# Optimization experiments

Measured on AMD Instinct MI355X. Metric: run time of the kernel, lower is better.

## Reference

```python
import jax, jax.numpy as jnp
import numpy as np

DIM = 96
SHIFT_SIZE = 3
EPS = 1e-5


def conv1x1(x, w, b):
    # x: [B,C,H,W], w: [O,C], b: [O]
    return jnp.einsum('bchw,oc->bohw', x, w) + b[None, :, None, None]


def group_norm1(x, gamma, beta):
    # GroupNorm with 1 group: normalize over (C,H,W) per sample
    mean = jnp.mean(x, axis=(1, 2, 3), keepdims=True)
    var = jnp.var(x, axis=(1, 2, 3), keepdims=True)
    xn = (x - mean) * jax.lax.rsqrt(var + EPS)
    return xn * gamma[None, :, None, None] + beta[None, :, None, None]


def axial_shift(x, shift_size, axis, sign=1):
    # pad -> chunk channels -> roll each chunk -> cat -> narrow (zero-fill shift)
    B, C, H, W = x.shape
    p = shift_size // 2
    xp = jnp.pad(x, ((0, 0), (0, 0), (p, p), (p, p)))
    chunks = jnp.split(xp, shift_size, axis=1)
    rolled = [jnp.roll(c, sign * s, axis=axis) for c, s in zip(chunks, range(-p, p + 1))]
    xc = jnp.concatenate(rolled, axis=1)
    return xc[:, :, p:p + H, p:p + W]


def setup_inputs() -> dict:
    key = jax.random.key(0)
    ks = jax.random.split(key, 13)
    B, C, H, W = 4, DIM, 256, 256
    s = 1.0 / np.sqrt(C)
    inp = {
        'x': jax.random.normal(ks[0], (B, C, H, W), jnp.float32),
        'w1': jax.random.uniform(ks[1], (C, C), jnp.float32, -s, s),
        'b1': jax.random.uniform(ks[2], (C,), jnp.float32, -s, s),
        'w21': jax.random.uniform(ks[3], (C, C), jnp.float32, -s, s),
        'b21': jax.random.uniform(ks[4], (C,), jnp.float32, -s, s),
        'w22': jax.random.uniform(ks[5], (C, C), jnp.float32, -s, s),
        'b22': jax.random.uniform(ks[6], (C,), jnp.float32, -s, s),
        'w3': jax.random.uniform(ks[7], (C, C), jnp.float32, -s, s),
        'b3': jax.random.uniform(ks[8], (C,), jnp.float32, -s, s),
        'gn1_w': jnp.ones((C,), jnp.float32),
        'gn1_b': jnp.zeros((C,), jnp.float32),
        'gn2_w': jnp.ones((C,), jnp.float32),
        'gn2_b': jnp.zeros((C,), jnp.float32),
    }
    return inp


def reference(x, w1, b1, w21, b21, w22, b22, w3, b3, gn1_w, gn1_b, gn2_w, gn2_b):
    gelu = lambda t: jax.nn.gelu(t, approximate=False)  # torch nn.GELU default (erf)
    x = gelu(group_norm1(conv1x1(x, w1, b1), gn1_w, gn1_b))
    x_lr = axial_shift(x, SHIFT_SIZE, axis=3)
    x_l_diag = axial_shift(x_lr, SHIFT_SIZE, axis=2)
    x_td = axial_shift(x, SHIFT_SIZE, axis=2)
    x_r_diag = axial_shift(x_td, SHIFT_SIZE, axis=3, sign=-1)
    out = (gelu(conv1x1(x_lr, w21, b21)) + gelu(conv1x1(x_l_diag, w21, b21))
           + gelu(conv1x1(x_td, w22, b22)) + gelu(conv1x1(x_r_diag, w22, b22)))
    out = group_norm1(out, gn2_w, gn2_b)
    return conv1x1(out, w3, b3)
```

## Files before the change

kernel.cpp:

```cpp
#include <hip/hip_runtime.h>
#include <hip/hip_bf16.h>
#include <math.h>


#define B_ 4
#define C_ 96
#define H_ 256
#define W_ 256
#define NPIX (H_ * W_)
#define GN_N ((float)(C_ * NPIX))
#define CPAD 104

#define HT 8
#define WT 16
#define HHT (HT + 2)
#define HWT (WT + 2)
#define HALO_PX (HHT * HWT)
#define GR_PX 12
#define ROW_GR (HWT * GR_PX)
#define TOT_GR (HHT * ROW_GR)

typedef __attribute__((ext_vector_type(4))) float f32x4;
typedef __attribute__((ext_vector_type(8))) short short8;
typedef __attribute__((ext_vector_type(2))) unsigned int uint2v;
typedef __attribute__((ext_vector_type(4))) unsigned int uint4v;

__device__ __forceinline__ float bf2f(unsigned short u) {
    return __uint_as_float(((unsigned int)u) << 16);
}
__device__ __forceinline__ unsigned short f2bf(float v) {
    unsigned int u = __float_as_uint(v);
    unsigned int r = (u + 0x7FFFu + ((u >> 16) & 1u)) >> 16;
    return (unsigned short)r;
}
__device__ __forceinline__ unsigned int cvtpk(float lo, float hi) {
    unsigned int r;
    asm("v_cvt_pk_bf16_f32 %0, %1, %2" : "=v"(r) : "v"(lo), "v"(hi));
    return r;
}

__device__ __forceinline__ float gelu_f(float v) {
    float t = fmaf(v * v, 0.1029433f, 2.3021178f);
    float e = __builtin_amdgcn_exp2f(v * t);
    float r = __builtin_amdgcn_rcpf(e + 1.0f);
    return v - v * r;
}

__device__ __forceinline__ float waveReduceSum(float v) {
#pragma unroll
    for (int off = 32; off > 0; off >>= 1) v += __shfl_down(v, off);
    return v;
}

__device__ __forceinline__ f32x4 mfma16(short8 a, short8 b, f32x4 c) {
    return __builtin_amdgcn_mfma_f32_16x16x32_bf16(a, b, c, 0, 0, 0);
}

__global__ void k0_prep(const float* __restrict__ w1, const float* __restrict__ w21,
                        const float* __restrict__ w22, const float* __restrict__ w3,
                        unsigned short* __restrict__ wb, float* __restrict__ stats) {
    int t = blockIdx.x * 256 + threadIdx.x;
    if (blockIdx.x == 0 && threadIdx.x < 16) stats[threadIdx.x] = 0.f;
    if (t >= 4 * C_ * C_) return;
    int m = t / (C_ * C_);
    int r = t - m * (C_ * C_);
    const float* src = (m == 0) ? w1 : (m == 1) ? w21 : (m == 2) ? w22 : w3;
    wb[t] = f2bf(src[r]);
}

__global__ __launch_bounds__(256, 3) void k1_conv1(
    const float* __restrict__ x, const unsigned short* __restrict__ w1b,
    const float* __restrict__ b1, unsigned short* __restrict__ ap,
    float* __restrict__ stats) {
    __shared__ unsigned short xs[256 * CPAD];
    __shared__ float red[8];
    int tid = threadIdx.x;
    int b = blockIdx.x >> 8;
    int h = blockIdx.x & 255;
    int pix0 = h << 8;
    size_t xbase = (size_t)b * C_ * NPIX + pix0 + tid;
    int lb = tid * CPAD;
#pragma unroll
    for (int c0 = 0; c0 < C_; c0 += 8) {
        float f[8];
#pragma unroll
        for (int j = 0; j < 8; ++j) f[j] = x[xbase + (size_t)(c0 + j) * NPIX];
        uint4v pk = {cvtpk(f[0], f[1]), cvtpk(f[2], f[3]),
                     cvtpk(f[4], f[5]), cvtpk(f[6], f[7])};
        *reinterpret_cast<uint4v*>(&xs[lb + c0]) = pk;
    }
    __syncthreads();
    int l = tid & 63, wv = tid >> 6;
    int bx = l & 15, q = l >> 4, cl = q * 8;
    short8 bfr[4][3];
#pragma unroll
    for (int nf = 0; nf < 4; ++nf) {
        int p = (4 * wv + nf) * 16 + bx;
#pragma unroll
        for (int kb = 0; kb < 3; ++kb)
            bfr[nf][kb] = *reinterpret_cast<const short8*>(&xs[p * CPAD + kb * 32 + cl]);
    }
    unsigned int* xsu = reinterpret_cast<unsigned int*>(xs);
    float ls = 0.f, lsq = 0.f;
    for (int mt = 0; mt < 6; ++mt) {
        int m0 = mt * 16;
        const unsigned short* wp = w1b + (m0 + bx) * C_ + cl;
        short8 af[3];
#pragma unroll
        for (int kb = 0; kb < 3; ++kb)
            af[kb] = *reinterpret_cast<const short8*>(wp + kb * 32);
        f32x4 acc[4];
#pragma unroll
        for (int nf = 0; nf < 4; ++nf) acc[nf] = (f32x4){0.f, 0.f, 0.f, 0.f};
#pragma unroll
        for (int nf = 0; nf < 4; ++nf)
#pragma unroll
            for (int kb = 0; kb < 3; ++kb)
                acc[nf] = mfma16(af[kb], bfr[nf][kb], acc[nf]);
        int o = m0 + q * 4;
        float b0 = b1[o], b1v = b1[o + 1], b2v = b1[o + 2], b3v = b1[o + 3];
#pragma unroll
        for (int nf = 0; nf < 4; ++nf) {
            int p = (4 * wv + nf) * 16 + bx;
            float y0 = acc[nf][0] + b0, y1v = acc[nf][1] + b1v;
            float y2 = acc[nf][2] + b2v, y3 = acc[nf][3] + b3v;
            ls += y0 + y1v + y2 + y3;
            lsq += y0 * y0 + y1v * y1v + y2 * y2 + y3 * y3;
            xsu[p * (CPAD / 2) + (o >> 1)] = cvtpk(y0, y1v);
            xsu[p * (CPAD / 2) + (o >> 1) + 1] = cvtpk(y2, y3);
        }
    }
    __syncthreads();
    size_t abase = (size_t)(b * NPIX + pix0 + tid) * C_;
#pragma unroll
    for (int c0 = 0; c0 < C_; c0 += 8)
        *reinterpret_cast<short8*>(&ap[abase + c0]) =
            *reinterpret_cast<short8*>(&xs[tid * CPAD + c0]);
    ls = waveReduceSum(ls);
    lsq = waveReduceSum(lsq);
    if (l == 0) { red[wv] = ls; red[4 + wv] = lsq; }
    __syncthreads();
    if (tid == 0) {
        atomicAdd(&stats[b], red[0] + red[1] + red[2] + red[3]);
        atomicAdd(&stats[4 + b], red[4] + red[5] + red[6] + red[7]);
    }
}

__global__ void k2_fin(float* stats, int so, int dof) {
    int t = threadIdx.x;
    if (t < 4) {
        float mean = stats[so + t] / GN_N;
        float var = stats[so + 4 + t] / GN_N - mean * mean;
        stats[dof + t] = mean;
        stats[dof + 4 + t] = rsqrtf(var + 1e-5f);
    }
}

__global__ __launch_bounds__(512, 6) void k3_main(
    const unsigned short* __restrict__ ap,
    const unsigned short* __restrict__ w21b, const float* __restrict__ b21,
    const unsigned short* __restrict__ w22b, const float* __restrict__ b22,
    const float* __restrict__ gn1w, const float* __restrict__ gn1b,
    unsigned short* __restrict__ zb, float* __restrict__ stats) {
    __shared__ unsigned short as_t[HALO_PX * CPAD];
    __shared__ float red[16];
    __shared__ float scs[C_], offs[C_];
    int tid = threadIdx.x;
    int wseg = blockIdx.x & 15;
    int hseg = (blockIdx.x >> 4) & 31;
    int b = blockIdx.x >> 9;
    int l = tid & 63, wv = tid >> 6;
    int h0 = hseg * HT, w0 = wseg * WT;
    float m1 = stats[16 + b], r1 = stats[20 + b];
    if (tid < C_) {
        float sc = r1 * gn1w[tid];
        scs[tid] = sc;
        offs[tid] = gn1b[tid] - m1 * sc;
    }
    __syncthreads();
    for (int g = tid; g < TOT_GR; g += 512) {
        int row = g / ROW_GR;
        int rem = g - row * ROW_GR;
        int p = rem / GR_PX;
        int cgr = rem - p * GR_PX;
        int hh = h0 - 1 + row, ww = w0 - 1 + p;
        unsigned short* dst = &as_t[(row * HWT + p) * CPAD + cgr * 8];
        if (((unsigned)hh < (unsigned)H_) && ((unsigned)ww < (unsigned)W_)) {
            short8 raw = *reinterpret_cast<const short8*>(
                &ap[(size_t)(b * NPIX + hh * W_ + ww) * C_ + cgr * 8]);
            float gv[8];
#pragma unroll
            for (int j = 0; j < 8; ++j) {
                int c = cgr * 8 + j;
                gv[j] = gelu_f(fmaf(bf2f((unsigned short)raw[j]), scs[c], offs[c]));
            }
            uint4v pk = {cvtpk(gv[0], gv[1]), cvtpk(gv[2], gv[3]),
                         cvtpk(gv[4], gv[5]), cvtpk(gv[6], gv[7])};
            *reinterpret_cast<uint4v*>(dst) = pk;
        } else {
            *reinterpret_cast<uint4v*>(dst) = (uint4v){0, 0, 0, 0};
        }
    }
    __syncthreads();
    int bx = l & 15, q = l >> 4, cl = q * 8;
    int Xb = (bx + 1) * CPAD + cl;
#define FR(R, dx, kb) (*reinterpret_cast<const short8*>( \
        &as_t[((R)*HWT + (dx)) * CPAD + Xb + (kb)*32]))
    float ls = 0.f, lsq = 0.f;
    {
        int r = wv;
        short8 f0a = FR(r + 1, 1, 0), f0b = FR(r + 2, 1, 0);
        short8 f0c = FR(r + 2, 0, 0), f0d = FR(r + 2, -1, 0);
        short8 fC = FR(r + 1, 0, 1);
        short8 f2a = FR(r + 1, -1, 2), f2b = FR(r, -1, 2);
        short8 f2c = FR(r, 0, 2), f2d = FR(r, 1, 2);
        size_t zpix = (size_t)(b * NPIX + (h0 + r) * W_ + w0 + bx) * C_;
        for (int mt = 0; mt < 6; ++mt) {
            int m0 = mt * 16;
            const unsigned short* wpa = w21b + (m0 + bx) * C_ + cl;
            const unsigned short* wpb = w22b + (m0 + bx) * C_ + cl;
            short8 aA0 = *reinterpret_cast<const short8*>(wpa);
            short8 aA1 = *reinterpret_cast<const short8*>(wpa + 32);
            short8 aA2 = *reinterpret_cast<const short8*>(wpa + 64);
            short8 aB0 = *reinterpret_cast<const short8*>(wpb);
            short8 aB1 = *reinterpret_cast<const short8*>(wpb + 32);
            short8 aB2 = *reinterpret_cast<const short8*>(wpb + 64);
            const f32x4 bb1 = *reinterpret_cast<const f32x4*>(&b21[m0 + q * 4]);
            const f32x4 bb2 = *reinterpret_cast<const f32x4*>(&b22[m0 + q * 4]);
            f32x4 a0 = bb1, a1 = bb1, a2 = bb2, a3 = bb2;
            a0 = mfma16(aA0, f0a, a0);
            a1 = mfma16(aA0, f0b, a1);
            a2 = mfma16(aB0, f0c, a2);
            a3 = mfma16(aB0, f0d, a3);
            a0 = mfma16(aA1, fC, a0);
            a1 = mfma16(aA1, fC, a1);
            a2 = mfma16(aB1, fC, a2);
            a3 = mfma16(aB1, fC, a3);
            a0 = mfma16(aA2, f2a, a0);
            a1 = mfma16(aA2, f2b, a1);
            a2 = mfma16(aB2, f2c, a2);
            a3 = mfma16(aB2, f2d, a3);
            float zv[4];
#pragma unroll
            for (int rg = 0; rg < 4; ++rg) {
                float z0 = gelu_f(a0[rg]) + gelu_f(a1[rg]) +
                           gelu_f(a2[rg]) + gelu_f(a3[rg]);
                zv[rg] = z0;
                ls += z0;
                lsq += z0 * z0;
            }
            uint2v pk;
            pk.x = cvtpk(zv[0], zv[1]);
            pk.y = cvtpk(zv[2], zv[3]);
            *reinterpret_cast<uint2v*>(&zb[zpix + m0 + q * 4]) = pk;
        }
    }
#undef FR
    ls = waveReduceSum(ls);
    lsq = waveReduceSum(lsq);
    if (l == 0) { red[wv] = ls; red[8 + wv] = lsq; }
    __syncthreads();
    if (tid == 0) {
        float s0 = 0.f, s1 = 0.f;
#pragma unroll
        for (int i = 0; i < 8; ++i) { s0 += red[i]; s1 += red[8 + i]; }
        atomicAdd(&stats[8 + b], s0);
        atomicAdd(&stats[12 + b], s1);
    }
}

__global__ void k4b_fold(const float* __restrict__ w3, const float* __restrict__ b3,
                         const float* __restrict__ gn2w, const float* __restrict__ gn2b,
                         const float* __restrict__ stats,
                         unsigned short* __restrict__ w3p, float* __restrict__ b3p) {
    int b = blockIdx.x;
    int o = threadIdx.x;
    float mean = stats[8 + b] / GN_N;
    float var = stats[12 + b] / GN_N - mean * mean;
    float r2 = rsqrtf(var + 1e-5f);
    float acc = 0.f;
    for (int c = 0; c < C_; ++c) {
        float sc = r2 * gn2w[c];
        float off = gn2b[c] - mean * sc;
        float wv = w3[o * C_ + c];
        acc = fmaf(wv, off, acc);
        w3p[((size_t)b * C_ + o) * C_ + c] = f2bf(wv * sc);
    }
    b3p[b * C_ + o] = acc + b3[o];
}

__global__ __launch_bounds__(256, 3) void k5_conv3(
    const unsigned short* __restrict__ zb,
    const unsigned short* __restrict__ w3p, const float* __restrict__ b3p,
    float* __restrict__ out) {
    __shared__ unsigned short zs[256 * CPAD];
    int tid = threadIdx.x;
    int b = blockIdx.x >> 8;
    int pix0 = (blockIdx.x & 255) << 8;
    {
        const short8* src = reinterpret_cast<const short8*>(
            &zb[(size_t)(b * NPIX + pix0 + tid) * C_]);
        int lb = tid * CPAD;
#pragma unroll
        for (int i = 0; i < 12; ++i)
            *reinterpret_cast<short8*>(&zs[lb + i * 8]) = src[i];
    }
    __syncthreads();
    int l = tid & 63, wv = tid >> 6;
    int bx = l & 15, q = l >> 4, cl = q * 8;
    short8 bfr[4][3];
#pragma unroll
    for (int nf = 0; nf < 4; ++nf) {
        int p = (4 * wv + nf) * 16 + bx;
#pragma unroll
        for (int kb = 0; kb < 3; ++kb)
            bfr[nf][kb] = *reinterpret_cast<const short8*>(&zs[p * CPAD + kb * 32 + cl]);
    }
    const unsigned short* wbase = w3p + (size_t)b * C_ * C_;
    const float* bb = b3p + b * C_;
    for (int mt = 0; mt < 6; ++mt) {
        int m0 = mt * 16;
        const unsigned short* wp = wbase + (m0 + bx) * C_ + cl;
        short8 af0 = *reinterpret_cast<const short8*>(wp);
        short8 af1 = *reinterpret_cast<const short8*>(wp + 32);
        short8 af2 = *reinterpret_cast<const short8*>(wp + 64);
        f32x4 acc[4];
#pragma unroll
        for (int nf = 0; nf < 4; ++nf) acc[nf] = (f32x4){0.f, 0.f, 0.f, 0.f};
#pragma unroll
        for (int nf = 0; nf < 4; ++nf) {
            acc[nf] = mfma16(af0, bfr[nf][0], acc[nf]);
            acc[nf] = mfma16(af1, bfr[nf][1], acc[nf]);
            acc[nf] = mfma16(af2, bfr[nf][2], acc[nf]);
        }
        int o = m0 + q * 4;
        float b0 = bb[o], b1v = bb[o + 1], b2v = bb[o + 2], b3v = bb[o + 3];
#pragma unroll
        for (int nf = 0; nf < 4; ++nf) {
            int p = pix0 + (4 * wv + nf) * 16 + bx;
            size_t ob0 = (size_t)(b * C_ + o) * NPIX + p;
            out[ob0] = acc[nf][0] + b0;
            out[ob0 + NPIX] = acc[nf][1] + b1v;
            out[ob0 + 2 * NPIX] = acc[nf][2] + b2v;
            out[ob0 + 3 * NPIX] = acc[nf][3] + b3v;
        }
    }
}

extern "C" void kernel_launch(void* const* d_in, const int* in_sizes, int n_in,
                              void* d_out, int out_size, void* d_ws, size_t ws_size,
                              hipStream_t stream) {
    const float* x = (const float*)d_in[0];
    const float* w1 = (const float*)d_in[1];
    const float* b1 = (const float*)d_in[2];
    const float* w21 = (const float*)d_in[3];
    const float* b21 = (const float*)d_in[4];
    const float* w22 = (const float*)d_in[5];
    const float* b22 = (const float*)d_in[6];
    const float* w3 = (const float*)d_in[7];
    const float* b3 = (const float*)d_in[8];
    const float* gn1w = (const float*)d_in[9];
    const float* gn1b = (const float*)d_in[10];
    const float* gn2w = (const float*)d_in[11];
    const float* gn2b = (const float*)d_in[12];
    float* out = (float*)d_out;
    char* ws = (char*)d_ws;

    const size_t NB = (size_t)B_ * NPIX * C_ * sizeof(unsigned short);
    unsigned short* ap = (unsigned short*)ws;
    unsigned short* zb = (unsigned short*)(ws + NB);
    float* stats = (float*)(ws + 2 * NB);
    unsigned short* wb = (unsigned short*)(ws + 2 * NB + 128);
    unsigned short* w1b = wb;
    unsigned short* w21b = wb + C_ * C_;
    unsigned short* w22b = wb + 2 * C_ * C_;
    unsigned short* w3p = wb + 4 * C_ * C_;
    float* b3p = (float*)(w3p + B_ * C_ * C_);

    hipLaunchKernelGGL(k0_prep, dim3(144), dim3(256), 0, stream,
                       w1, w21, w22, w3, wb, stats);
    hipLaunchKernelGGL(k1_conv1, dim3(1024), dim3(256), 0, stream, x, w1b, b1, ap, stats);
    hipLaunchKernelGGL(k2_fin, dim3(1), dim3(64), 0, stream, stats, 0, 16);
    hipLaunchKernelGGL(k3_main, dim3(2048), dim3(512), 0, stream,
                       ap, w21b, b21, w22b, b22, gn1w, gn1b, zb, stats);
    hipLaunchKernelGGL(k4b_fold, dim3(B_), dim3(C_), 0, stream,
                       w3, b3, gn2w, gn2b, stats, w3p, b3p);
    hipLaunchKernelGGL(k5_conv3, dim3(1024), dim3(256), 0, stream,
                       zb, w3p, b3p, out);
}
```

Measured before the change: 176.7 us.

## Coalesce global stores/loads of NHWC tiles via LDS staging and halve k3 block size

The k1 and k5 global copies of the channel-last activation tiles are remapped so consecutive threads touch consecutive 16-byte chunks, instead of each thread streaming its own 192-byte pixel. In k3 the block shrinks from 512 to 256 threads, with each wave computing two rows and keeping the packed results in registers. Those results are then written back through the shared halo buffer and stored to global memory in a coalesced pattern. The change targets uncoalesced memory traffic, at the cost of extra syncthreads, more registers in k3 and different occupancy.

Result: slower. 294.2 us (+66.5%).

```diff
diff --git a/kernel.cpp b/kernel.cpp
--- a/kernel.cpp
+++ b/kernel.cpp
@@ -131,11 +131,16 @@
         }
     }
     __syncthreads();
-    size_t abase = (size_t)(b * NPIX + pix0 + tid) * C_;
-#pragma unroll
-    for (int c0 = 0; c0 < C_; c0 += 8)
-        *reinterpret_cast<short8*>(&ap[abase + c0]) =
-            *reinterpret_cast<short8*>(&xs[tid * CPAD + c0]);
+    {
+        size_t gb = (size_t)(b * NPIX + pix0) * C_;
+#pragma unroll
+        for (int k = 0; k < 12; ++k) {
+            int g = tid + k * 256;
+            int pix = g / 12, cgr = g - pix * 12;
+            *reinterpret_cast<short8*>(&ap[gb + (size_t)g * 8]) =
+                *reinterpret_cast<short8*>(&xs[pix * CPAD + cgr * 8]);
+        }
+    }
     ls = waveReduceSum(ls);
     lsq = waveReduceSum(lsq);
     if (l == 0) { red[wv] = ls; red[4 + wv] = lsq; }
@@ -156,14 +161,14 @@
     }
 }
 
-__global__ __launch_bounds__(512, 6) void k3_main(
+__global__ __launch_bounds__(256, 4) void k3_main(
     const unsigned short* __restrict__ ap,
     const unsigned short* __restrict__ w21b, const float* __restrict__ b21,
     const unsigned short* __restrict__ w22b, const float* __restrict__ b22,
     const float* __restrict__ gn1w, const float* __restrict__ gn1b,
     unsigned short* __restrict__ zb, float* __restrict__ stats) {
     __shared__ unsigned short as_t[HALO_PX * CPAD];
-    __shared__ float red[16];
+    __shared__ float red[8];
     __shared__ float scs[C_], offs[C_];
     int tid = threadIdx.x;
     int wseg = blockIdx.x & 15;
@@ -178,7 +183,7 @@
         offs[tid] = gn1b[tid] - m1 * sc;
     }
     __syncthreads();
-    for (int g = tid; g < TOT_GR; g += 512) {
+    for (int g = tid; g < TOT_GR; g += 256) {
         int row = g / ROW_GR;
         int rem = g - row * ROW_GR;
         int p = rem / GR_PX;
@@ -207,14 +212,16 @@
 #define FR(R, dx, kb) (*reinterpret_cast<const short8*>( \
         &as_t[((R)*HWT + (dx)) * CPAD + Xb + (kb)*32]))
     float ls = 0.f, lsq = 0.f;
-    {
-        int r = wv;
+    uint2v zp[2][6];
+#pragma unroll
+    for (int nf = 0; nf < 2; ++nf) {
+        int r = 2 * wv + nf;
         short8 f0a = FR(r + 1, 1, 0), f0b = FR(r + 2, 1, 0);
         short8 f0c = FR(r + 2, 0, 0), f0d = FR(r + 2, -1, 0);
         short8 fC = FR(r + 1, 0, 1);
         short8 f2a = FR(r + 1, -1, 2), f2b = FR(r, -1, 2);
         short8 f2c = FR(r, 0, 2), f2d = FR(r, 1, 2);
-        size_t zpix = (size_t)(b * NPIX + (h0 + r) * W_ + w0 + bx) * C_;
+#pragma unroll
         for (int mt = 0; mt < 6; ++mt) {
             int m0 = mt * 16;
             const unsigned short* wpa = w21b + (m0 + bx) * C_ + cl;
@@ -249,23 +256,36 @@
                 ls += z0;
                 lsq += z0 * z0;
             }
-            uint2v pk;
-            pk.x = cvtpk(zv[0], zv[1]);
-            pk.y = cvtpk(zv[2], zv[3]);
-            *reinterpret_cast<uint2v*>(&zb[zpix + m0 + q * 4]) = pk;
+            zp[nf][mt].x = cvtpk(zv[0], zv[1]);
+            zp[nf][mt].y = cvtpk(zv[2], zv[3]);
         }
     }
 #undef FR
+    __syncthreads();
+#pragma unroll
+    for (int nf = 0; nf < 2; ++nf) {
+        int p = (2 * wv + nf) * WT + bx;
+#pragma unroll
+        for (int mt = 0; mt < 6; ++mt)
+            *reinterpret_cast<uint2v*>(&as_t[p * CPAD + mt * 16 + q * 4]) = zp[nf][mt];
+    }
+    __syncthreads();
+#pragma unroll
+    for (int k = 0; k < 6; ++k) {
+        int g = tid + k * 256;
+        int pix = g / 12, cgr = g - pix * 12;
+        int row = pix >> 4, col = pix & 15;
+        size_t addr = (size_t)(b * NPIX + (h0 + row) * W_ + w0 + col) * C_ + cgr * 8;
+        *reinterpret_cast<short8*>(&zb[addr]) =
+            *reinterpret_cast<short8*>(&as_t[pix * CPAD + cgr * 8]);
+    }
     ls = waveReduceSum(ls);
     lsq = waveReduceSum(lsq);
-    if (l == 0) { red[wv] = ls; red[8 + wv] = lsq; }
+    if (l == 0) { red[wv] = ls; red[4 + wv] = lsq; }
     __syncthreads();
     if (tid == 0) {
-        float s0 = 0.f, s1 = 0.f;
-#pragma unroll
-        for (int i = 0; i < 8; ++i) { s0 += red[i]; s1 += red[8 + i]; }
-        atomicAdd(&stats[8 + b], s0);
-        atomicAdd(&stats[12 + b], s1);
+        atomicAdd(&stats[8 + b], red[0] + red[1] + red[2] + red[3]);
+        atomicAdd(&stats[12 + b], red[4] + red[5] + red[6] + red[7]);
     }
 }
 
@@ -298,12 +318,14 @@
     int b = blockIdx.x >> 8;
     int pix0 = (blockIdx.x & 255) << 8;
     {
-        const short8* src = reinterpret_cast<const short8*>(
-            &zb[(size_t)(b * NPIX + pix0 + tid) * C_]);
-        int lb = tid * CPAD;
-#pragma unroll
-        for (int i = 0; i < 12; ++i)
-            *reinterpret_cast<short8*>(&zs[lb + i * 8]) = src[i];
+        size_t gb = (size_t)(b * NPIX + pix0) * C_;
+#pragma unroll
+        for (int k = 0; k < 12; ++k) {
+            int g = tid + k * 256;
+            int pix = g / 12, cgr = g - pix * 12;
+            *reinterpret_cast<short8*>(&zs[pix * CPAD + cgr * 8]) =
+                *reinterpret_cast<const short8*>(&zb[gb + (size_t)g * 8]);
+        }
     }
     __syncthreads();
     int l = tid & 63, wv = tid >> 6;
@@ -381,7 +403,7 @@
                        w1, w21, w22, w3, wb, stats);
     hipLaunchKernelGGL(k1_conv1, dim3(1024), dim3(256), 0, stream, x, w1b, b1, ap, stats);
     hipLaunchKernelGGL(k2_fin, dim3(1), dim3(64), 0, stream, stats, 0, 16);
-    hipLaunchKernelGGL(k3_main, dim3(2048), dim3(512), 0, stream,
+    hipLaunchKernelGGL(k3_main, dim3(2048), dim3(256), 0, stream,
                        ap, w21b, b21, w22b, b22, gn1w, gn1b, zb, stats);
     hipLaunchKernelGGL(k4b_fold, dim3(B_), dim3(C_), 0, stream,
                        w3, b3, gn2w, gn2b, stats, w3p, b3p);
```

## Pre-swizzle weights into MFMA fragment order and halve k3 block size

Applied to the files above, without the earlier changes.

Weights are reordered during prep (and in the GN2 fold) into MFMA A-fragment order, so each lane loads its short8 fragment from a contiguous, coalesced address instead of strided rows. k3_main moves from 512 threads with one row per wave to 256 threads with two rows per wave, which reuses the loaded weight fragments across two rows and changes occupancy. The fold kernel now uses 256 threads to write the swizzled w3. Running fewer waves per block may lower latency hiding in k3.

New measurement: 167.1 us. 5.4% less time.

```diff
diff --git a/kernel.cpp b/kernel.cpp
--- a/kernel.cpp
+++ b/kernel.cpp
@@ -10,6 +10,7 @@
 #define NPIX (H_ * W_)
 #define GN_N ((float)(C_ * NPIX))
 #define CPAD 104
+#define WFRAG 9216
 
 #define HT 8
 #define WT 16
@@ -56,20 +57,29 @@
     return __builtin_amdgcn_mfma_f32_16x16x32_bf16(a, b, c, 0, 0, 0);
 }
 
+__device__ __forceinline__ short8 wfrag(const unsigned short* __restrict__ wf,
+                                        int mt, int kb, int l) {
+    return *reinterpret_cast<const short8*>(wf + (((mt * 3 + kb) << 6) + l) * 8);
+}
+
 __global__ void k0_prep(const float* __restrict__ w1, const float* __restrict__ w21,
-                        const float* __restrict__ w22, const float* __restrict__ w3,
-                        unsigned short* __restrict__ wb, float* __restrict__ stats) {
+                        const float* __restrict__ w22,
+                        unsigned short* __restrict__ wf, float* __restrict__ stats) {
     int t = blockIdx.x * 256 + threadIdx.x;
     if (blockIdx.x == 0 && threadIdx.x < 16) stats[threadIdx.x] = 0.f;
-    if (t >= 4 * C_ * C_) return;
-    int m = t / (C_ * C_);
-    int r = t - m * (C_ * C_);
-    const float* src = (m == 0) ? w1 : (m == 1) ? w21 : (m == 2) ? w22 : w3;
-    wb[t] = f2bf(src[r]);
+    if (t >= 3 * WFRAG) return;
+    int m = t / WFRAG, rm = t - m * WFRAG;
+    int f = rm >> 3, j = rm & 7;
+    int mt = f / 192, rem = f - mt * 192;
+    int kb = rem >> 6, l = rem & 63;
+    int row = mt * 16 + (l & 15);
+    int col = kb * 32 + ((l >> 4) << 3) + j;
+    const float* src = (m == 0) ? w1 : (m == 1) ? w21 : w22;
+    wf[t] = f2bf(src[row * C_ + col]);
 }
 
 __global__ __launch_bounds__(256, 3) void k1_conv1(
-    const float* __restrict__ x, const unsigned short* __restrict__ w1b,
+    const float* __restrict__ x, const unsigned short* __restrict__ w1f,
     const float* __restrict__ b1, unsigned short* __restrict__ ap,
     float* __restrict__ stats) {
     __shared__ unsigned short xs[256 * CPAD];
@@ -104,11 +114,9 @@
     float ls = 0.f, lsq = 0.f;
     for (int mt = 0; mt < 6; ++mt) {
         int m0 = mt * 16;
-        const unsigned short* wp = w1b + (m0 + bx) * C_ + cl;
         short8 af[3];
 #pragma unroll
-        for (int kb = 0; kb < 3; ++kb)
-            af[kb] = *reinterpret_cast<const short8*>(wp + kb * 32);
+        for (int kb = 0; kb < 3; ++kb) af[kb] = wfrag(w1f, mt, kb, l);
         f32x4 acc[4];
 #pragma unroll
         for (int nf = 0; nf < 4; ++nf) acc[nf] = (f32x4){0.f, 0.f, 0.f, 0.f};
@@ -156,14 +164,14 @@
     }
 }
 
-__global__ __launch_bounds__(512, 6) void k3_main(
+__global__ __launch_bounds__(256, 4) void k3_main(
     const unsigned short* __restrict__ ap,
-    const unsigned short* __restrict__ w21b, const float* __restrict__ b21,
-    const unsigned short* __restrict__ w22b, const float* __restrict__ b22,
+    const unsigned short* __restrict__ w21f, const float* __restrict__ b21,
+    const unsigned short* __restrict__ w22f, const float* __restrict__ b22,
     const float* __restrict__ gn1w, const float* __restrict__ gn1b,
     unsigned short* __restrict__ zb, float* __restrict__ stats) {
     __shared__ unsigned short as_t[HALO_PX * CPAD];
-    __shared__ float red[16];
+    __shared__ float red[8];
     __shared__ float scs[C_], offs[C_];
     int tid = threadIdx.x;
     int wseg = blockIdx.x & 15;
@@ -178,7 +186,7 @@
         offs[tid] = gn1b[tid] - m1 * sc;
     }
     __syncthreads();
-    for (int g = tid; g < TOT_GR; g += 512) {
+    for (int g = tid; g < TOT_GR; g += 256) {
         int row = g / ROW_GR;
         int rem = g - row * ROW_GR;
         int p = rem / GR_PX;
@@ -207,8 +215,9 @@
 #define FR(R, dx, kb) (*reinterpret_cast<const short8*>( \
         &as_t[((R)*HWT + (dx)) * CPAD + Xb + (kb)*32]))
     float ls = 0.f, lsq = 0.f;
-    {
-        int r = wv;
+#pragma unroll
+    for (int nf = 0; nf < 2; ++nf) {
+        int r = 2 * wv + nf;
         short8 f0a = FR(r + 1, 1, 0), f0b = FR(r + 2, 1, 0);
         short8 f0c = FR(r + 2, 0, 0), f0d = FR(r + 2, -1, 0);
         short8 fC = FR(r + 1, 0, 1);
@@ -217,14 +226,12 @@
         size_t zpix = (size_t)(b * NPIX + (h0 + r) * W_ + w0 + bx) * C_;
         for (int mt = 0; mt < 6; ++mt) {
             int m0 = mt * 16;
-            const unsigned short* wpa = w21b + (m0 + bx) * C_ + cl;
-            const unsigned short* wpb = w22b + (m0 + bx) * C_ + cl;
-            short8 aA0 = *reinterpret_cast<const short8*>(wpa);
-            short8 aA1 = *reinterpret_cast<const short8*>(wpa + 32);
-            short8 aA2 = *reinterpret_cast<const short8*>(wpa + 64);
-            short8 aB0 = *reinterpret_cast<const short8*>(wpb);
-            short8 aB1 = *reinterpret_cast<const short8*>(wpb + 32);
-            short8 aB2 = *reinterpret_cast<const short8*>(wpb + 64);
+            short8 aA0 = wfrag(w21f, mt, 0, l);
+            short8 aA1 = wfrag(w21f, mt, 1, l);
+            short8 aA2 = wfrag(w21f, mt, 2, l);
+            short8 aB0 = wfrag(w22f, mt, 0, l);
+            short8 aB1 = wfrag(w22f, mt, 1, l);
+            short8 aB2 = wfrag(w22f, mt, 2, l);
             const f32x4 bb1 = *reinterpret_cast<const f32x4*>(&b21[m0 + q * 4]);
             const f32x4 bb2 = *reinterpret_cast<const f32x4*>(&b22[m0 + q * 4]);
             f32x4 a0 = bb1, a1 = bb1, a2 = bb2, a3 = bb2;
@@ -258,40 +265,48 @@
 #undef FR
     ls = waveReduceSum(ls);
     lsq = waveReduceSum(lsq);
-    if (l == 0) { red[wv] = ls; red[8 + wv] = lsq; }
+    if (l == 0) { red[wv] = ls; red[4 + wv] = lsq; }
     __syncthreads();
     if (tid == 0) {
-        float s0 = 0.f, s1 = 0.f;
-#pragma unroll
-        for (int i = 0; i < 8; ++i) { s0 += red[i]; s1 += red[8 + i]; }
-        atomicAdd(&stats[8 + b], s0);
-        atomicAdd(&stats[12 + b], s1);
+        atomicAdd(&stats[8 + b], red[0] + red[1] + red[2] + red[3]);
+        atomicAdd(&stats[12 + b], red[4] + red[5] + red[6] + red[7]);
     }
 }
 
 __global__ void k4b_fold(const float* __restrict__ w3, const float* __restrict__ b3,
                          const float* __restrict__ gn2w, const float* __restrict__ gn2b,
                          const float* __restrict__ stats,
-                         unsigned short* __restrict__ w3p, float* __restrict__ b3p) {
+                         unsigned short* __restrict__ w3pf, float* __restrict__ b3p) {
     int b = blockIdx.x;
-    int o = threadIdx.x;
+    int t = threadIdx.x;
     float mean = stats[8 + b] / GN_N;
     float var = stats[12 + b] / GN_N - mean * mean;
     float r2 = rsqrtf(var + 1e-5f);
-    float acc = 0.f;
-    for (int c = 0; c < C_; ++c) {
-        float sc = r2 * gn2w[c];
-        float off = gn2b[c] - mean * sc;
-        float wv = w3[o * C_ + c];
-        acc = fmaf(wv, off, acc);
-        w3p[((size_t)b * C_ + o) * C_ + c] = f2bf(wv * sc);
-    }
-    b3p[b * C_ + o] = acc + b3[o];
+#pragma unroll
+    for (int k = 0; k < 36; ++k) {
+        int idx = t + k * 256;
+        int f = idx >> 3, j = idx & 7;
+        int mt = f / 192, rem = f - mt * 192;
+        int kb = rem >> 6, l = rem & 63;
+        int row = mt * 16 + (l & 15);
+        int col = kb * 32 + ((l >> 4) << 3) + j;
+        float sc = r2 * gn2w[col];
+        w3pf[(size_t)b * WFRAG + idx] = f2bf(w3[row * C_ + col] * sc);
+    }
+    if (t < C_) {
+        float acc = 0.f;
+        for (int c = 0; c < C_; ++c) {
+            float sc = r2 * gn2w[c];
+            float off = gn2b[c] - mean * sc;
+            acc = fmaf(w3[t * C_ + c], off, acc);
+        }
+        b3p[b * C_ + t] = acc + b3[t];
+    }
 }
 
 __global__ __launch_bounds__(256, 3) void k5_conv3(
     const unsigned short* __restrict__ zb,
-    const unsigned short* __restrict__ w3p, const float* __restrict__ b3p,
+    const unsigned short* __restrict__ w3pf, const float* __restrict__ b3p,
     float* __restrict__ out) {
     __shared__ unsigned short zs[256 * CPAD];
     int tid = threadIdx.x;
@@ -316,14 +331,13 @@
         for (int kb = 0; kb < 3; ++kb)
             bfr[nf][kb] = *reinterpret_cast<const short8*>(&zs[p * CPAD + kb * 32 + cl]);
     }
-    const unsigned short* wbase = w3p + (size_t)b * C_ * C_;
+    const unsigned short* wbase = w3pf + (size_t)b * WFRAG;
     const float* bb = b3p + b * C_;
     for (int mt = 0; mt < 6; ++mt) {
         int m0 = mt * 16;
-        const unsigned short* wp = wbase + (m0 + bx) * C_ + cl;
-        short8 af0 = *reinterpret_cast<const short8*>(wp);
-        short8 af1 = *reinterpret_cast<const short8*>(wp + 32);
-        short8 af2 = *reinterpret_cast<const short8*>(wp + 64);
+        short8 af0 = wfrag(wbase, mt, 0, l);
+        short8 af1 = wfrag(wbase, mt, 1, l);
+        short8 af2 = wfrag(wbase, mt, 2, l);
         f32x4 acc[4];
 #pragma unroll
         for (int nf = 0; nf < 4; ++nf) acc[nf] = (f32x4){0.f, 0.f, 0.f, 0.f};
@@ -370,21 +384,21 @@
     unsigned short* ap = (unsigned short*)ws;
     unsigned short* zb = (unsigned short*)(ws + NB);
     float* stats = (float*)(ws + 2 * NB);
-    unsigned short* wb = (unsigned short*)(ws + 2 * NB + 128);
-    unsigned short* w1b = wb;
-    unsigned short* w21b = wb + C_ * C_;
-    unsigned short* w22b = wb + 2 * C_ * C_;
-    unsigned short* w3p = wb + 4 * C_ * C_;
-    float* b3p = (float*)(w3p + B_ * C_ * C_);
-
-    hipLaunchKernelGGL(k0_prep, dim3(144), dim3(256), 0, stream,
-                       w1, w21, w22, w3, wb, stats);
-    hipLaunchKernelGGL(k1_conv1, dim3(1024), dim3(256), 0, stream, x, w1b, b1, ap, stats);
+    unsigned short* wf = (unsigned short*)(ws + 2 * NB + 128);
+    unsigned short* w1f = wf;
+    unsigned short* w21f = wf + WFRAG;
+    unsigned short* w22f = wf + 2 * WFRAG;
+    unsigned short* w3pf = wf + 3 * WFRAG;
+    float* b3p = (float*)(w3pf + B_ * WFRAG);
+
+    hipLaunchKernelGGL(k0_prep, dim3(112), dim3(256), 0, stream,
+                       w1, w21, w22, wf, stats);
+    hipLaunchKernelGGL(k1_conv1, dim3(1024), dim3(256), 0, stream, x, w1f, b1, ap, stats);
     hipLaunchKernelGGL(k2_fin, dim3(1), dim3(64), 0, stream, stats, 0, 16);
-    hipLaunchKernelGGL(k3_main, dim3(2048), dim3(512), 0, stream,
-                       ap, w21b, b21, w22b, b22, gn1w, gn1b, zb, stats);
-    hipLaunchKernelGGL(k4b_fold, dim3(B_), dim3(C_), 0, stream,
-                       w3, b3, gn2w, gn2b, stats, w3p, b3p);
+    hipLaunchKernelGGL(k3_main, dim3(2048), dim3(256), 0, stream,
+                       ap, w21f, b21, w22f, b22, gn1w, gn1b, zb, stats);
+    hipLaunchKernelGGL(k4b_fold, dim3(B_), dim3(256), 0, stream,
+                       w3, b3, gn2w, gn2b, stats, w3pf, b3p);
     hipLaunchKernelGGL(k5_conv3, dim3(1024), dim3(256), 0, stream,
-                       zb, w3p, b3p, out);
-}
+                       zb, w3pf, b3p, out);
+}
```
